# Optimization experiments

Hardware: AMD Instinct MI355X
Metric: run time of the kernel (lower is better)

The kernel has to match this reference:

```python
import jax, jax.numpy as jnp
import numpy as np

N_NODES = 100000
N_EDGES = 800000
N_ETYPES = 5
IN_DIM = 23
HID_DIM = 128
OUT_DIM = 64
NUM_GRAPHS = 64


def setup_inputs() -> dict:
    key = jax.random.key(0)
    ks = jax.random.split(key, 8)
    feat = jax.random.normal(ks[0], (N_NODES, IN_DIM), dtype=jnp.float32)
    src = jax.random.randint(ks[1], (N_ETYPES, N_EDGES), 0, N_NODES, dtype=jnp.int32)
    dst = jax.random.randint(ks[2], (N_ETYPES, N_EDGES), 0, N_NODES, dtype=jnp.int32)
    graph_ids = jnp.sort(jax.random.randint(ks[3], (N_NODES,), 0, NUM_GRAPHS, dtype=jnp.int32))
    W1 = jax.random.normal(ks[4], (N_ETYPES, IN_DIM, HID_DIM), dtype=jnp.float32) * 0.1
    b1 = jnp.zeros((N_ETYPES, HID_DIM), dtype=jnp.float32)
    W2 = jax.random.normal(ks[5], (N_ETYPES, HID_DIM, OUT_DIM), dtype=jnp.float32) * 0.1
    b2 = jnp.zeros((N_ETYPES, OUT_DIM), dtype=jnp.float32)
    return {"feat": feat, "src": src, "dst": dst, "graph_ids": graph_ids,
            "W1": W1, "b1": b1, "W2": W2, "b2": b2}


def _hetero_sage_layer(h, src, dst, W, b):
    """HeteroGraphConv of SAGEConv(aggregator='gcn') summed over edge types.
    gcn aggregator: h_neigh[i] = (sum_{j->i} h[j] + h[i]) / (in_deg(i) + 1);
    per-etype output = h_neigh @ W_e + b_e; combine with sum."""
    n = h.shape[0]
    out = jnp.zeros((n, W.shape[-1]), dtype=h.dtype)
    ones_e = jnp.ones((src.shape[1],), dtype=h.dtype)
    for e in range(N_ETYPES):
        deg = jax.ops.segment_sum(ones_e, dst[e], num_segments=n)          # [N]
        agg = jax.ops.segment_sum(h[src[e]], dst[e], num_segments=n)       # [N, D]
        h_neigh = (agg + h) / (deg + 1.0)[:, None]
        out = out + h_neigh @ W[e] + b[e]
    return out


def reference(feat, src, dst, graph_ids, W1, b1, W2, b2):
    # layer 1: in_dim -> hid, relu (dropout in eval mode = identity)
    h = jax.nn.relu(_hetero_sage_layer(feat, src, dst, W1, b1))
    # layer 2: hid -> out (no activation)
    h = _hetero_sage_layer(h, src, dst, W2, b2)
    # dgl.mean_nodes: per-graph mean over nodes
    counts = jax.ops.segment_sum(jnp.ones((h.shape[0],), h.dtype), graph_ids,
                                 num_segments=NUM_GRAPHS)
    sums = jax.ops.segment_sum(h, graph_ids, num_segments=NUM_GRAPHS)
    return sums / jnp.maximum(counts, 1.0)[:, None]
```

## Files before the change

### kernel.cpp

```cpp
#include <hip/hip_runtime.h>

#define N_NODES   100000
#define N_EDGES   800000
#define N_ETYPES  5
#define IN_DIM    23
#define HID_DIM   128
#define OUT_DIM   64
#define NUM_GRAPHS 64
#define NBKT      391
#define PBLK      125
#define CHUNK     6400
#define NB_E      (N_ETYPES*NBKT)
#define BKT_CAP   3072
#define ASTR      136
#define A1STR     40


__device__ __forceinline__ unsigned short f2bf(float x) {
    unsigned u = __float_as_uint(x);
    unsigned r = (u + 0x7FFFu + ((u >> 16) & 1u)) >> 16;
    return (unsigned short)r;
}
__device__ __forceinline__ float bf2f(unsigned short h) {
    return __uint_as_float(((unsigned)h) << 16);
}

typedef __attribute__((ext_vector_type(8))) short bf16x8;
typedef __attribute__((ext_vector_type(4))) float f32x4;
typedef __attribute__((ext_vector_type(2))) float f32x2;

__global__ __launch_bounds__(256) void cvt_feat_k(const float* __restrict__ feat,
                                                  unsigned short* __restrict__ fb8) {
    int i = blockIdx.x * 256 + threadIdx.x;
    if (i < N_NODES * 16) {
        int n = i >> 4, p = i & 15;
        int d0 = p * 2, d1 = d0 + 1;
        float f0 = (d0 < IN_DIM) ? feat[n * IN_DIM + d0] : 0.f;
        float f1 = (d1 < IN_DIM) ? feat[n * IN_DIM + d1] : 0.f;
        int pk = __builtin_amdgcn_cvt_pk_fp8_f32(f0, f1, 0, false);
        fb8[i] = (unsigned short)(pk & 0xFFFF);
    }
}

__global__ __launch_bounds__(256) void cvt_w_k(const float* __restrict__ W1,
                                               const float* __restrict__ b1,
                                               const float* __restrict__ W2,
                                               unsigned short* __restrict__ w1tb,
                                               unsigned short* __restrict__ w2tb,
                                               float* __restrict__ b1s) {
    int i = blockIdx.x * 256 + threadIdx.x;
    if (i < N_ETYPES * OUT_DIM * HID_DIM) {
        int e = i / (OUT_DIM * HID_DIM);
        int r = i - e * (OUT_DIM * HID_DIM);
        int n = r >> 7, k = r & 127;
        w2tb[i] = f2bf(W2[(e * HID_DIM + k) * OUT_DIM + n]);
    }
    if (i < N_ETYPES * HID_DIM * 32) {
        int e = i / (HID_DIM * 32);
        int r = i - e * (HID_DIM * 32);
        int n = r >> 5, k = r & 31;
        w1tb[i] = (k < IN_DIM) ? f2bf(W1[e * IN_DIM * HID_DIM + k * HID_DIM + n])
                               : (unsigned short)0;
    }
    if (i < HID_DIM) {
        float s = 0.f;
        for (int e = 0; e < N_ETYPES; e++) s += b1[e * HID_DIM + i];
        b1s[i] = s;
    }
}

__global__ __launch_bounds__(256) void part_k(const int* __restrict__ src,
                                              const int* __restrict__ dst,
                                              int* __restrict__ gcur,
                                              unsigned* __restrict__ ep) {
    __shared__ int hist[NBKT];
    __shared__ int cur[NBKT];
    int e = blockIdx.y, blk = blockIdx.x, t = threadIdx.x;
    for (int b = t; b < NBKT; b += 256) hist[b] = 0;
    __syncthreads();
    const int* dp = dst + e * N_EDGES + blk * CHUNK;
    const int* sp = src + e * N_EDGES + blk * CHUNK;
    for (int k = t; k < CHUNK; k += 256) atomicAdd(&hist[dp[k] >> 8], 1);
    __syncthreads();
    for (int b = t; b < NBKT; b += 256)
        cur[b] = (hist[b] > 0) ? atomicAdd(&gcur[e * NBKT + b], hist[b]) : 0;
    __syncthreads();
    for (int k = t; k < CHUNK; k += 256) {
        int d = dp[k], s = sp[k];
        int b = d >> 8;
        int pos = atomicAdd(&cur[b], 1);
        if (pos < BKT_CAP)
            ep[(size_t)(e * NBKT + b) * BKT_CAP + pos] =
                (unsigned)s | ((unsigned)(d & 255) << 24);
    }
}

__global__ __launch_bounds__(256) void sort_k(const int* __restrict__ gcur,
                                              const unsigned* __restrict__ ep,
                                              unsigned* __restrict__ csr,
                                              int* __restrict__ noff,
                                              int* __restrict__ degn,
                                              float* __restrict__ inv) {
    __shared__ unsigned recs[BKT_CAP];
    __shared__ int hist[256];
    __shared__ int scn[256];
    __shared__ int curp[256];
    int b = blockIdx.x, e = blockIdx.y, t = threadIdx.x;
    int lin = e * NBKT + b;
    int S = lin * BKT_CAP;
    int cnt = gcur[lin];
    if (cnt > BKT_CAP) cnt = BKT_CAP;
    hist[t] = 0;
    __syncthreads();
    for (int i = t; i < cnt; i += 256) {
        unsigned r = ep[S + i];
        recs[i] = r;
        atomicAdd(&hist[r >> 24], 1);
    }
    __syncthreads();
    scn[t] = hist[t];
    __syncthreads();
    for (int o = 1; o < 256; o <<= 1) {
        int x = (t >= o) ? scn[t - o] : 0;
        __syncthreads();
        scn[t] += x;
        __syncthreads();
    }
    int excl = scn[t] - hist[t];
    curp[t] = excl;
    int n = b * 256 + t;
    if (n < N_NODES) {
        noff[e * N_NODES + n] = S + excl;
        degn[e * N_NODES + n] = hist[t];
        inv[e * N_NODES + n]  = 1.f / (float)(hist[t] + 1);
    }
    __syncthreads();
    for (int i = t; i < cnt; i += 256) {
        unsigned r = recs[i];
        int pos = atomicAdd(&curp[r >> 24], 1);
        csr[S + pos] = r & 0xFFFFFFu;
    }
}

__global__ __launch_bounds__(256) void agg1_k(const int* __restrict__ noff,
                                              const int* __restrict__ degn,
                                              const unsigned* __restrict__ csr,
                                              const unsigned short* __restrict__ fb8,
                                              const float* __restrict__ inv,
                                              unsigned short* __restrict__ agg1b) {
    int e = blockIdx.y;
    int t = threadIdx.x;
    int lane = t & 15;
    int n = blockIdx.x * 16 + (t >> 4);
    int idx = e * N_NODES + n;
    int st = noff[idx];
    int cnt = degn[idx];
    f32x2 sv = __builtin_amdgcn_cvt_pk_f32_fp8((int)fb8[n * 16 + lane], false);
    float a0 = sv.x, a1 = sv.y;
    int k = 0;
    for (; k + 3 < cnt; k += 4) {
        int s0 = csr[st + k];
        int s1 = csr[st + k + 1];
        int s2 = csr[st + k + 2];
        int s3 = csr[st + k + 3];
        unsigned short r0 = fb8[s0 * 16 + lane];
        unsigned short r1 = fb8[s1 * 16 + lane];
        unsigned short r2 = fb8[s2 * 16 + lane];
        unsigned short r3 = fb8[s3 * 16 + lane];
        f32x2 v0 = __builtin_amdgcn_cvt_pk_f32_fp8((int)r0, false);
        f32x2 v1 = __builtin_amdgcn_cvt_pk_f32_fp8((int)r1, false);
        f32x2 v2 = __builtin_amdgcn_cvt_pk_f32_fp8((int)r2, false);
        f32x2 v3 = __builtin_amdgcn_cvt_pk_f32_fp8((int)r3, false);
        a0 += (v0.x + v1.x) + (v2.x + v3.x);
        a1 += (v0.y + v1.y) + (v2.y + v3.y);
    }
    for (; k < cnt; k++) {
        int s0 = csr[st + k];
        f32x2 v0 = __builtin_amdgcn_cvt_pk_f32_fp8((int)fb8[s0 * 16 + lane], false);
        a0 += v0.x;
        a1 += v0.y;
    }
    float iv = inv[idx];
    ushort2 o; o.x = f2bf(a0 * iv); o.y = f2bf(a1 * iv);
    *(ushort2*)&agg1b[(size_t)idx * 32 + lane * 2] = o;
}

__global__ __launch_bounds__(256) void gemm12_k(const unsigned short* __restrict__ agg1b,
                                                const unsigned short* __restrict__ w1tb,
                                                const float* __restrict__ b1s,
                                                const unsigned short* __restrict__ w2tb,
                                                unsigned char* __restrict__ t2f8) {
    __shared__ unsigned short H1s[64 * ASTR];
    __shared__ unsigned short Wt2[64 * ASTR];
    unsigned short* As1 = Wt2;
    unsigned short* Wt1 = Wt2 + 64 * A1STR;
    int t = threadIdx.x;
    int node0 = blockIdx.x * 64;
    int w = t >> 6, lane = t & 63;
    int m = lane & 15, quad = lane >> 4;

    f32x4 acc[8];
    for (int nt = 0; nt < 8; nt++) {
        float bb = b1s[nt * 16 + m];
        f32x4 c = {bb, bb, bb, bb};
        acc[nt] = c;
    }
    for (int e = 0; e < N_ETYPES; e++) {
        __syncthreads();
        for (int j = t; j < 64 * 8; j += 256) {
            int n = j >> 3, c4 = (j & 7) * 4;
            int gn = node0 + n;
            int cn = gn < N_NODES ? gn : N_NODES - 1;
            *(ushort4*)&As1[n * A1STR + c4] =
                *(const ushort4*)&agg1b[(size_t)(e * N_NODES + cn) * 32 + c4];
        }
        for (int j = t; j < 128 * 8; j += 256) {
            int n = j >> 3, c4 = (j & 7) * 4;
            *(ushort4*)&Wt1[n * A1STR + c4] =
                *(const ushort4*)&w1tb[(size_t)(e * HID_DIM + n) * 32 + c4];
        }
        __syncthreads();
        bf16x8 a = *(const bf16x8*)&As1[(w * 16 + m) * A1STR + quad * 8];
        for (int nt = 0; nt < 8; nt++) {
            bf16x8 b = *(const bf16x8*)&Wt1[(nt * 16 + m) * A1STR + quad * 8];
            acc[nt] = __builtin_amdgcn_mfma_f32_16x16x32_bf16(a, b, acc[nt], 0, 0, 0);
        }
    }
    __syncthreads();
    for (int nt = 0; nt < 8; nt++)
        for (int r = 0; r < 4; r++)
            H1s[(w * 16 + quad * 4 + r) * ASTR + nt * 16 + m] =
                f2bf(fmaxf(acc[nt][r], 0.f));
    __syncthreads();

    bf16x8 a2[4];
    for (int ks = 0; ks < 4; ks++)
        a2[ks] = *(const bf16x8*)&H1s[(w * 16 + m) * ASTR + ks * 32 + quad * 8];
    for (int e = 0; e < N_ETYPES; e++) {
        __syncthreads();
        for (int j = t; j < 64 * 32; j += 256) {
            int n = j >> 5, c4 = (j & 31) * 4;
            *(ushort4*)&Wt2[n * ASTR + c4] =
                *(const ushort4*)&w2tb[(e * OUT_DIM + n) * HID_DIM + c4];
        }
        __syncthreads();
        unsigned char* out = t2f8 + (size_t)e * N_NODES * OUT_DIM;
        for (int nt = 0; nt < 4; nt++) {
            f32x4 c = {0.f, 0.f, 0.f, 0.f};
            for (int ks = 0; ks < 4; ks++) {
                bf16x8 b = *(const bf16x8*)&Wt2[(nt * 16 + m) * ASTR + ks * 32 + quad * 8];
                c = __builtin_amdgcn_mfma_f32_16x16x32_bf16(a2[ks], b, c, 0, 0, 0);
            }
            for (int r = 0; r < 4; r++) {
                int gn = node0 + w * 16 + quad * 4 + r;
                if (gn < N_NODES) {
                    int p = __builtin_amdgcn_cvt_pk_fp8_f32(c[r], c[r], 0, false);
                    out[(size_t)gn * OUT_DIM + nt * 16 + m] = (unsigned char)(p & 0xFF);
                }
            }
        }
    }
}

__global__ __launch_bounds__(256) void gather2_k(const int* __restrict__ noff,
                                                 const int* __restrict__ degn,
                                                 const float* __restrict__ inv,
                                                 const unsigned* __restrict__ csr,
                                                 const unsigned char* __restrict__ t2f8,
                                                 const int* __restrict__ gid,
                                                 float* __restrict__ gsum) {
    __shared__ float4 red4[16 * 4 * 16];
    int b = blockIdx.x, qb = blockIdx.y, t = threadIdx.x;
    int lane = t & 15, ng = t >> 4;
    int nbase = b * 256 + qb * 32;
    int gbase = nbase < N_NODES ? nbase : N_NODES - 1;
    int g0 = gid[gbase];
    float4 f[2];
    f[0] = make_float4(0.f, 0.f, 0.f, 0.f);
    f[1] = make_float4(0.f, 0.f, 0.f, 0.f);

    for (int e = 0; e < N_ETYPES; e++) {
        const unsigned char* base = t2f8 + (size_t)e * N_NODES * OUT_DIM;
        #pragma unroll
        for (int pass = 0; pass < 2; pass++) {
            int n = nbase + pass * 16 + ng;
            if (n >= N_NODES) break;
            int idx = e * N_NODES + n;
            int st = noff[idx];
            int cnt = degn[idx];
            float iv = inv[idx];
            unsigned rv = *(const unsigned*)&base[(size_t)n * OUT_DIM + lane * 4];
            f32x2 lo = __builtin_amdgcn_cvt_pk_f32_fp8((int)rv, false);
            f32x2 hi = __builtin_amdgcn_cvt_pk_f32_fp8((int)rv, true);
            float ax = lo.x, ay = lo.y, az = hi.x, aw = hi.y;
            int k = 0;
            for (; k + 3 < cnt; k += 4) {
                int sA = csr[st + k];
                int sB = csr[st + k + 1];
                int sC = csr[st + k + 2];
                int sD = csr[st + k + 3];
                unsigned rA = *(const unsigned*)&base[(size_t)sA * OUT_DIM + lane * 4];
                unsigned rB = *(const unsigned*)&base[(size_t)sB * OUT_DIM + lane * 4];
                unsigned rC = *(const unsigned*)&base[(size_t)sC * OUT_DIM + lane * 4];
                unsigned rD = *(const unsigned*)&base[(size_t)sD * OUT_DIM + lane * 4];
                f32x2 lA = __builtin_amdgcn_cvt_pk_f32_fp8((int)rA, false);
                f32x2 hA = __builtin_amdgcn_cvt_pk_f32_fp8((int)rA, true);
                f32x2 lB = __builtin_amdgcn_cvt_pk_f32_fp8((int)rB, false);
                f32x2 hB = __builtin_amdgcn_cvt_pk_f32_fp8((int)rB, true);
                f32x2 lC = __builtin_amdgcn_cvt_pk_f32_fp8((int)rC, false);
                f32x2 hC = __builtin_amdgcn_cvt_pk_f32_fp8((int)rC, true);
                f32x2 lD = __builtin_amdgcn_cvt_pk_f32_fp8((int)rD, false);
                f32x2 hD = __builtin_amdgcn_cvt_pk_f32_fp8((int)rD, true);
                ax += (lA.x + lB.x) + (lC.x + lD.x);
                ay += (lA.y + lB.y) + (lC.y + lD.y);
                az += (hA.x + hB.x) + (hC.x + hD.x);
                aw += (hA.y + hB.y) + (hC.y + hD.y);
            }
            for (; k < cnt; k++) {
                int sA = csr[st + k];
                unsigned rA = *(const unsigned*)&base[(size_t)sA * OUT_DIM + lane * 4];
                f32x2 lA = __builtin_amdgcn_cvt_pk_f32_fp8((int)rA, false);
                f32x2 hA = __builtin_amdgcn_cvt_pk_f32_fp8((int)rA, true);
                ax += lA.x; ay += lA.y; az += hA.x; aw += hA.y;
            }
            f[pass].x += iv * ax; f[pass].y += iv * ay;
            f[pass].z += iv * az; f[pass].w += iv * aw;
        }
    }

    float4 sa0 = {0,0,0,0}, sa1 = {0,0,0,0}, sa2 = {0,0,0,0}, sa3 = {0,0,0,0};
    #pragma unroll
    for (int pass = 0; pass < 2; pass++) {
        int n = nbase + pass * 16 + ng;
        if (n >= N_NODES) break;
        float4 v = f[pass];
        int slot = gid[n] - g0;
        float m0 = (slot == 0) ? 1.f : 0.f;
        float m1 = (slot == 1) ? 1.f : 0.f;
        float m2 = (slot == 2) ? 1.f : 0.f;
        float m3 = (slot == 3) ? 1.f : 0.f;
        sa0.x += m0 * v.x; sa0.y += m0 * v.y; sa0.z += m0 * v.z; sa0.w += m0 * v.w;
        sa1.x += m1 * v.x; sa1.y += m1 * v.y; sa1.z += m1 * v.z; sa1.w += m1 * v.w;
        sa2.x += m2 * v.x; sa2.y += m2 * v.y; sa2.z += m2 * v.z; sa2.w += m2 * v.w;
        sa3.x += m3 * v.x; sa3.y += m3 * v.y; sa3.z += m3 * v.z; sa3.w += m3 * v.w;
        if (slot > 3) {
            atomicAdd(&gsum[(g0 + slot) * 64 + lane * 4 + 0], v.x);
            atomicAdd(&gsum[(g0 + slot) * 64 + lane * 4 + 1], v.y);
            atomicAdd(&gsum[(g0 + slot) * 64 + lane * 4 + 2], v.z);
            atomicAdd(&gsum[(g0 + slot) * 64 + lane * 4 + 3], v.w);
        }
    }
    red4[(ng * 4 + 0) * 16 + lane] = sa0;
    red4[(ng * 4 + 1) * 16 + lane] = sa1;
    red4[(ng * 4 + 2) * 16 + lane] = sa2;
    red4[(ng * 4 + 3) * 16 + lane] = sa3;
    __syncthreads();
    const float* red = (const float*)red4;
    int slot = t >> 6, d = t & 63;
    float s = 0.f;
    for (int j = 0; j < 16; j++) s += red[(j * 4 + slot) * 64 + d];
    int g = g0 + slot;
    if (g < NUM_GRAPHS) atomicAdd(&gsum[g * 64 + d], s);
}

__global__ __launch_bounds__(256) void gcnt_k(const int* __restrict__ gid,
                                              float* __restrict__ gcnt) {
    __shared__ int h[NUM_GRAPHS];
    int b = blockIdx.x, t = threadIdx.x;
    if (t < NUM_GRAPHS) h[t] = 0;
    __syncthreads();
    int n = b * 256 + t;
    if (n < N_NODES) atomicAdd(&h[gid[n]], 1);
    __syncthreads();
    if (t < NUM_GRAPHS && h[t] > 0) atomicAdd(&gcnt[t], (float)h[t]);
}

__global__ __launch_bounds__(256) void final_k(const float* __restrict__ gsum,
                                               const float* __restrict__ gcnt,
                                               const float* __restrict__ b2,
                                               float* __restrict__ out) {
    int idx = blockIdx.x * 256 + threadIdx.x;
    if (idx >= NUM_GRAPHS * OUT_DIM) return;
    int d = idx & 63;
    float B2 = 0.f;
    for (int e = 0; e < N_ETYPES; e++) B2 += b2[e * OUT_DIM + d];
    float c = gcnt[idx >> 6];
    out[idx] = (gsum[idx] + c * B2) / fmaxf(c, 1.0f);
}

extern "C" void kernel_launch(void* const* d_in, const int* in_sizes, int n_in,
                              void* d_out, int out_size, void* d_ws, size_t ws_size,
                              hipStream_t stream) {
    const float* feat = (const float*)d_in[0];
    const int*   src  = (const int*)d_in[1];
    const int*   dst  = (const int*)d_in[2];
    const int*   gid  = (const int*)d_in[3];
    const float* W1   = (const float*)d_in[4];
    const float* b1   = (const float*)d_in[5];
    const float* W2   = (const float*)d_in[6];
    const float* b2   = (const float*)d_in[7];

    float* ws = (float*)d_ws;
    int*            GCUR = (int*)ws;
    float*          INV  = ws + 2048;
    int*            NOFF = (int*)ws + 502048;
    int*            DEGN = (int*)ws + 1002048;
    unsigned short* FB8  = (unsigned short*)(ws + 1502048);
    float*          GSUM = ws + 2302048;
    float*          GCNT = ws + 2306144;
    unsigned*       EP   = (unsigned*)(ws + 2306208);
    unsigned*       CSR  = (unsigned*)(ws + 8311968);
    unsigned short* AGG1B= (unsigned short*)(ws + 14317728);
    unsigned char*  T2F8 = (unsigned char*)(ws + 22317728);
    unsigned short* W1TB = (unsigned short*)(ws + 30317728);
    unsigned short* W2TB = (unsigned short*)(ws + 30327968);
    float*          B1S  = ws + 30348448;

    hipMemsetAsync(GCUR, 0, 2048 * sizeof(int), stream);
    hipMemsetAsync(GSUM, 0, (size_t)(4096 + 64) * sizeof(float), stream);

    cvt_feat_k<<<(N_NODES * 16 + 255) / 256, 256, 0, stream>>>(feat, FB8);
    cvt_w_k<<<(N_ETYPES * OUT_DIM * HID_DIM + 255) / 256, 256, 0, stream>>>(
        W1, b1, W2, W1TB, W2TB, B1S);
    part_k<<<dim3(PBLK, N_ETYPES), 256, 0, stream>>>(src, dst, GCUR, EP);
    sort_k<<<dim3(NBKT, N_ETYPES), 256, 0, stream>>>(GCUR, EP, CSR, NOFF, DEGN, INV);

    agg1_k<<<dim3(6250, N_ETYPES), 256, 0, stream>>>(NOFF, DEGN, CSR, FB8, INV, AGG1B);
    gemm12_k<<<(N_NODES + 63) / 64, 256, 0, stream>>>(AGG1B, W1TB, B1S, W2TB, T2F8);
    gather2_k<<<dim3(NBKT, 8), 256, 0, stream>>>(NOFF, DEGN, INV, CSR, T2F8, gid, GSUM);

    gcnt_k<<<391, 256, 0, stream>>>(gid, GCNT);
    final_k<<<16, 256, 0, stream>>>(GSUM, GCNT, b2, (float*)d_out);
}
```

Baseline: 385.7 us.

## Fuse layer-1 neighbor aggregation into the GEMM kernel, dropping AGG1B buffer

Removes the separate agg1_k kernel and performs the fp8 feature gather and mean directly into shared memory inside gemm12_k, per edge type. This eliminates writing and re-reading the bf16 aggregated buffer (5×100k×32 bf16) and one kernel launch. In exchange, the gather latency now sits inside the GEMM kernel with only 1563 blocks, each 16-thread group serially handling 4 nodes, so latency hiding and parallelism for the irregular gather are reduced.

```diff
diff --git a/kernel.cpp b/kernel.cpp
--- a/kernel.cpp
+++ b/kernel.cpp
@@ -142,50 +142,11 @@
     }
 }
 
-__global__ __launch_bounds__(256) void agg1_k(const int* __restrict__ noff,
-                                              const int* __restrict__ degn,
-                                              const unsigned* __restrict__ csr,
-                                              const unsigned short* __restrict__ fb8,
-                                              const float* __restrict__ inv,
-                                              unsigned short* __restrict__ agg1b) {
-    int e = blockIdx.y;
-    int t = threadIdx.x;
-    int lane = t & 15;
-    int n = blockIdx.x * 16 + (t >> 4);
-    int idx = e * N_NODES + n;
-    int st = noff[idx];
-    int cnt = degn[idx];
-    f32x2 sv = __builtin_amdgcn_cvt_pk_f32_fp8((int)fb8[n * 16 + lane], false);
-    float a0 = sv.x, a1 = sv.y;
-    int k = 0;
-    for (; k + 3 < cnt; k += 4) {
-        int s0 = csr[st + k];
-        int s1 = csr[st + k + 1];
-        int s2 = csr[st + k + 2];
-        int s3 = csr[st + k + 3];
-        unsigned short r0 = fb8[s0 * 16 + lane];
-        unsigned short r1 = fb8[s1 * 16 + lane];
-        unsigned short r2 = fb8[s2 * 16 + lane];
-        unsigned short r3 = fb8[s3 * 16 + lane];
-        f32x2 v0 = __builtin_amdgcn_cvt_pk_f32_fp8((int)r0, false);
-        f32x2 v1 = __builtin_amdgcn_cvt_pk_f32_fp8((int)r1, false);
-        f32x2 v2 = __builtin_amdgcn_cvt_pk_f32_fp8((int)r2, false);
-        f32x2 v3 = __builtin_amdgcn_cvt_pk_f32_fp8((int)r3, false);
-        a0 += (v0.x + v1.x) + (v2.x + v3.x);
-        a1 += (v0.y + v1.y) + (v2.y + v3.y);
-    }
-    for (; k < cnt; k++) {
-        int s0 = csr[st + k];
-        f32x2 v0 = __builtin_amdgcn_cvt_pk_f32_fp8((int)fb8[s0 * 16 + lane], false);
-        a0 += v0.x;
-        a1 += v0.y;
-    }
-    float iv = inv[idx];
-    ushort2 o; o.x = f2bf(a0 * iv); o.y = f2bf(a1 * iv);
-    *(ushort2*)&agg1b[(size_t)idx * 32 + lane * 2] = o;
-}
-
-__global__ __launch_bounds__(256) void gemm12_k(const unsigned short* __restrict__ agg1b,
+__global__ __launch_bounds__(256) void gemm12_k(const int* __restrict__ noff,
+                                                const int* __restrict__ degn,
+                                                const float* __restrict__ inv,
+                                                const unsigned* __restrict__ csr,
+                                                const unsigned short* __restrict__ fb8,
                                                 const unsigned short* __restrict__ w1tb,
                                                 const float* __restrict__ b1s,
                                                 const unsigned short* __restrict__ w2tb,
@@ -198,6 +159,7 @@
     int node0 = blockIdx.x * 64;
     int w = t >> 6, lane = t & 63;
     int m = lane & 15, quad = lane >> 4;
+    int glane = t & 15, grp = t >> 4;
 
     f32x4 acc[8];
     for (int nt = 0; nt < 8; nt++) {
@@ -207,12 +169,37 @@
     }
     for (int e = 0; e < N_ETYPES; e++) {
         __syncthreads();
-        for (int j = t; j < 64 * 8; j += 256) {
-            int n = j >> 3, c4 = (j & 7) * 4;
-            int gn = node0 + n;
+        for (int i = 0; i < 4; i++) {
+            int nl = grp * 4 + i;
+            int gn = node0 + nl;
             int cn = gn < N_NODES ? gn : N_NODES - 1;
-            *(ushort4*)&As1[n * A1STR + c4] =
-                *(const ushort4*)&agg1b[(size_t)(e * N_NODES + cn) * 32 + c4];
+            int idx = e * N_NODES + cn;
+            int st = noff[idx];
+            int cnt = degn[idx];
+            float iv = inv[idx];
+            f32x2 sv = __builtin_amdgcn_cvt_pk_f32_fp8((int)fb8[cn * 16 + glane], false);
+            float a0 = sv.x, a1 = sv.y;
+            int k = 0;
+            for (; k + 3 < cnt; k += 4) {
+                int s0 = csr[st + k];
+                int s1 = csr[st + k + 1];
+                int s2 = csr[st + k + 2];
+                int s3 = csr[st + k + 3];
+                f32x2 v0 = __builtin_amdgcn_cvt_pk_f32_fp8((int)fb8[s0 * 16 + glane], false);
+                f32x2 v1 = __builtin_amdgcn_cvt_pk_f32_fp8((int)fb8[s1 * 16 + glane], false);
+                f32x2 v2 = __builtin_amdgcn_cvt_pk_f32_fp8((int)fb8[s2 * 16 + glane], false);
+                f32x2 v3 = __builtin_amdgcn_cvt_pk_f32_fp8((int)fb8[s3 * 16 + glane], false);
+                a0 += (v0.x + v1.x) + (v2.x + v3.x);
+                a1 += (v0.y + v1.y) + (v2.y + v3.y);
+            }
+            for (; k < cnt; k++) {
+                int s0 = csr[st + k];
+                f32x2 v0 = __builtin_amdgcn_cvt_pk_f32_fp8((int)fb8[s0 * 16 + glane], false);
+                a0 += v0.x;
+                a1 += v0.y;
+            }
+            ushort2 o; o.x = f2bf(a0 * iv); o.y = f2bf(a1 * iv);
+            *(ushort2*)&As1[nl * A1STR + glane * 2] = o;
         }
         for (int j = t; j < 128 * 8; j += 256) {
             int n = j >> 3, c4 = (j & 7) * 4;
@@ -410,11 +397,10 @@
     float*          GCNT = ws + 2306144;
     unsigned*       EP   = (unsigned*)(ws + 2306208);
     unsigned*       CSR  = (unsigned*)(ws + 8311968);
-    unsigned short* AGG1B= (unsigned short*)(ws + 14317728);
-    unsigned char*  T2F8 = (unsigned char*)(ws + 22317728);
-    unsigned short* W1TB = (unsigned short*)(ws + 30317728);
-    unsigned short* W2TB = (unsigned short*)(ws + 30327968);
-    float*          B1S  = ws + 30348448;
+    unsigned char*  T2F8 = (unsigned char*)(ws + 14317728);
+    unsigned short* W1TB = (unsigned short*)(ws + 22317728);
+    unsigned short* W2TB = (unsigned short*)(ws + 22327968);
+    float*          B1S  = ws + 22348448;
 
     hipMemsetAsync(GCUR, 0, 2048 * sizeof(int), stream);
     hipMemsetAsync(GSUM, 0, (size_t)(4096 + 64) * sizeof(float), stream);
@@ -425,8 +411,8 @@
     part_k<<<dim3(PBLK, N_ETYPES), 256, 0, stream>>>(src, dst, GCUR, EP);
     sort_k<<<dim3(NBKT, N_ETYPES), 256, 0, stream>>>(GCUR, EP, CSR, NOFF, DEGN, INV);
 
-    agg1_k<<<dim3(6250, N_ETYPES), 256, 0, stream>>>(NOFF, DEGN, CSR, FB8, INV, AGG1B);
-    gemm12_k<<<(N_NODES + 63) / 64, 256, 0, stream>>>(AGG1B, W1TB, B1S, W2TB, T2F8);
+    gemm12_k<<<(N_NODES + 63) / 64, 256, 0, stream>>>(NOFF, DEGN, INV, CSR, FB8,
+                                                      W1TB, B1S, W2TB, T2F8);
     gather2_k<<<dim3(NBKT, 8), 256, 0, stream>>>(NOFF, DEGN, INV, CSR, T2F8, gid, GSUM);
 
     gcnt_k<<<391, 256, 0, stream>>>(gid, GCNT);
```

New measurement: 401.3 us. +4.1%, slower.

## Fuse layer-1 neighbor aggregation into bucket sort kernel and merge conversion kernels

Applied to the files above, without the earlier changes.

The per-bucket sort kernel now keeps the sorted source indices in shared memory and runs the layer-1 fp8 feature aggregation for its 256 destination nodes right away, instead of launching a separate aggregation kernel that reloads CSR offsets, degrees and indices from global memory. The feature and weight conversion kernels are merged into one launch. This removes two launches and the global reads of CSR, offsets and degrees in the aggregation step. In exchange, parallelism for aggregation drops from 31250 blocks to 1955 blocks, and the extra shared-memory array may lower occupancy.

```diff
diff --git a/kernel.cpp b/kernel.cpp
--- a/kernel.cpp
+++ b/kernel.cpp
@@ -29,8 +29,14 @@
 typedef __attribute__((ext_vector_type(4))) float f32x4;
 typedef __attribute__((ext_vector_type(2))) float f32x2;
 
-__global__ __launch_bounds__(256) void cvt_feat_k(const float* __restrict__ feat,
-                                                  unsigned short* __restrict__ fb8) {
+__global__ __launch_bounds__(256) void cvt_k(const float* __restrict__ feat,
+                                             const float* __restrict__ W1,
+                                             const float* __restrict__ b1,
+                                             const float* __restrict__ W2,
+                                             unsigned short* __restrict__ fb8,
+                                             unsigned short* __restrict__ w1tb,
+                                             unsigned short* __restrict__ w2tb,
+                                             float* __restrict__ b1s) {
     int i = blockIdx.x * 256 + threadIdx.x;
     if (i < N_NODES * 16) {
         int n = i >> 4, p = i & 15;
@@ -40,15 +46,6 @@
         int pk = __builtin_amdgcn_cvt_pk_fp8_f32(f0, f1, 0, false);
         fb8[i] = (unsigned short)(pk & 0xFFFF);
     }
-}
-
-__global__ __launch_bounds__(256) void cvt_w_k(const float* __restrict__ W1,
-                                               const float* __restrict__ b1,
-                                               const float* __restrict__ W2,
-                                               unsigned short* __restrict__ w1tb,
-                                               unsigned short* __restrict__ w2tb,
-                                               float* __restrict__ b1s) {
-    int i = blockIdx.x * 256 + threadIdx.x;
     if (i < N_ETYPES * OUT_DIM * HID_DIM) {
         int e = i / (OUT_DIM * HID_DIM);
         int r = i - e * (OUT_DIM * HID_DIM);
@@ -95,16 +92,21 @@
     }
 }
 
-__global__ __launch_bounds__(256) void sort_k(const int* __restrict__ gcur,
-                                              const unsigned* __restrict__ ep,
-                                              unsigned* __restrict__ csr,
-                                              int* __restrict__ noff,
-                                              int* __restrict__ degn,
-                                              float* __restrict__ inv) {
+__global__ __launch_bounds__(256) void aggsort_k(const int* __restrict__ gcur,
+                                                 const unsigned* __restrict__ ep,
+                                                 unsigned* __restrict__ csr,
+                                                 int* __restrict__ noff,
+                                                 int* __restrict__ degn,
+                                                 float* __restrict__ inv,
+                                                 const unsigned short* __restrict__ fb8,
+                                                 unsigned short* __restrict__ agg1b) {
     __shared__ unsigned recs[BKT_CAP];
+    __shared__ unsigned srt[BKT_CAP];
     __shared__ int hist[256];
     __shared__ int scn[256];
     __shared__ int curp[256];
+    __shared__ int boffl[256];
+    __shared__ float invl[256];
     int b = blockIdx.x, e = blockIdx.y, t = threadIdx.x;
     int lin = e * NBKT + b;
     int S = lin * BKT_CAP;
@@ -128,61 +130,58 @@
     }
     int excl = scn[t] - hist[t];
     curp[t] = excl;
+    boffl[t] = excl;
+    float iv = 1.f / (float)(hist[t] + 1);
+    invl[t] = iv;
     int n = b * 256 + t;
     if (n < N_NODES) {
         noff[e * N_NODES + n] = S + excl;
         degn[e * N_NODES + n] = hist[t];
-        inv[e * N_NODES + n]  = 1.f / (float)(hist[t] + 1);
+        inv[e * N_NODES + n]  = iv;
     }
     __syncthreads();
     for (int i = t; i < cnt; i += 256) {
         unsigned r = recs[i];
         int pos = atomicAdd(&curp[r >> 24], 1);
-        csr[S + pos] = r & 0xFFFFFFu;
-    }
-}
-
-__global__ __launch_bounds__(256) void agg1_k(const int* __restrict__ noff,
-                                              const int* __restrict__ degn,
-                                              const unsigned* __restrict__ csr,
-                                              const unsigned short* __restrict__ fb8,
-                                              const float* __restrict__ inv,
-                                              unsigned short* __restrict__ agg1b) {
-    int e = blockIdx.y;
-    int t = threadIdx.x;
-    int lane = t & 15;
-    int n = blockIdx.x * 16 + (t >> 4);
-    int idx = e * N_NODES + n;
-    int st = noff[idx];
-    int cnt = degn[idx];
-    f32x2 sv = __builtin_amdgcn_cvt_pk_f32_fp8((int)fb8[n * 16 + lane], false);
-    float a0 = sv.x, a1 = sv.y;
-    int k = 0;
-    for (; k + 3 < cnt; k += 4) {
-        int s0 = csr[st + k];
-        int s1 = csr[st + k + 1];
-        int s2 = csr[st + k + 2];
-        int s3 = csr[st + k + 3];
-        unsigned short r0 = fb8[s0 * 16 + lane];
-        unsigned short r1 = fb8[s1 * 16 + lane];
-        unsigned short r2 = fb8[s2 * 16 + lane];
-        unsigned short r3 = fb8[s3 * 16 + lane];
-        f32x2 v0 = __builtin_amdgcn_cvt_pk_f32_fp8((int)r0, false);
-        f32x2 v1 = __builtin_amdgcn_cvt_pk_f32_fp8((int)r1, false);
-        f32x2 v2 = __builtin_amdgcn_cvt_pk_f32_fp8((int)r2, false);
-        f32x2 v3 = __builtin_amdgcn_cvt_pk_f32_fp8((int)r3, false);
-        a0 += (v0.x + v1.x) + (v2.x + v3.x);
-        a1 += (v0.y + v1.y) + (v2.y + v3.y);
-    }
-    for (; k < cnt; k++) {
-        int s0 = csr[st + k];
-        f32x2 v0 = __builtin_amdgcn_cvt_pk_f32_fp8((int)fb8[s0 * 16 + lane], false);
-        a0 += v0.x;
-        a1 += v0.y;
-    }
-    float iv = inv[idx];
-    ushort2 o; o.x = f2bf(a0 * iv); o.y = f2bf(a1 * iv);
-    *(ushort2*)&agg1b[(size_t)idx * 32 + lane * 2] = o;
+        srt[pos] = r & 0xFFFFFFu;
+    }
+    __syncthreads();
+    for (int i = t; i < cnt; i += 256) csr[S + i] = srt[i];
+
+    int glane = t & 15, grp = t >> 4;
+    for (int pass = 0; pass < 16; pass++) {
+        int nl = pass * 16 + grp;
+        int gn = b * 256 + nl;
+        int cn = gn < N_NODES ? gn : N_NODES - 1;
+        int st = boffl[nl];
+        int dn = hist[nl];
+        f32x2 sv = __builtin_amdgcn_cvt_pk_f32_fp8((int)fb8[cn * 16 + glane], false);
+        float a0 = sv.x, a1 = sv.y;
+        int k = 0;
+        for (; k + 3 < dn; k += 4) {
+            int s0 = srt[st + k];
+            int s1 = srt[st + k + 1];
+            int s2 = srt[st + k + 2];
+            int s3 = srt[st + k + 3];
+            f32x2 v0 = __builtin_amdgcn_cvt_pk_f32_fp8((int)fb8[s0 * 16 + glane], false);
+            f32x2 v1 = __builtin_amdgcn_cvt_pk_f32_fp8((int)fb8[s1 * 16 + glane], false);
+            f32x2 v2 = __builtin_amdgcn_cvt_pk_f32_fp8((int)fb8[s2 * 16 + glane], false);
+            f32x2 v3 = __builtin_amdgcn_cvt_pk_f32_fp8((int)fb8[s3 * 16 + glane], false);
+            a0 += (v0.x + v1.x) + (v2.x + v3.x);
+            a1 += (v0.y + v1.y) + (v2.y + v3.y);
+        }
+        for (; k < dn; k++) {
+            int s0 = srt[st + k];
+            f32x2 v0 = __builtin_amdgcn_cvt_pk_f32_fp8((int)fb8[s0 * 16 + glane], false);
+            a0 += v0.x;
+            a1 += v0.y;
+        }
+        if (gn < N_NODES) {
+            float ivv = invl[nl];
+            ushort2 o; o.x = f2bf(a0 * ivv); o.y = f2bf(a1 * ivv);
+            *(ushort2*)&agg1b[(size_t)(e * N_NODES + gn) * 32 + glane * 2] = o;
+        }
+    }
 }
 
 __global__ __launch_bounds__(256) void gemm12_k(const unsigned short* __restrict__ agg1b,
@@ -419,13 +418,11 @@
     hipMemsetAsync(GCUR, 0, 2048 * sizeof(int), stream);
     hipMemsetAsync(GSUM, 0, (size_t)(4096 + 64) * sizeof(float), stream);
 
-    cvt_feat_k<<<(N_NODES * 16 + 255) / 256, 256, 0, stream>>>(feat, FB8);
-    cvt_w_k<<<(N_ETYPES * OUT_DIM * HID_DIM + 255) / 256, 256, 0, stream>>>(
-        W1, b1, W2, W1TB, W2TB, B1S);
+    cvt_k<<<(N_NODES * 16 + 255) / 256, 256, 0, stream>>>(feat, W1, b1, W2,
+                                                          FB8, W1TB, W2TB, B1S);
     part_k<<<dim3(PBLK, N_ETYPES), 256, 0, stream>>>(src, dst, GCUR, EP);
-    sort_k<<<dim3(NBKT, N_ETYPES), 256, 0, stream>>>(GCUR, EP, CSR, NOFF, DEGN, INV);
-
-    agg1_k<<<dim3(6250, N_ETYPES), 256, 0, stream>>>(NOFF, DEGN, CSR, FB8, INV, AGG1B);
+    aggsort_k<<<dim3(NBKT, N_ETYPES), 256, 0, stream>>>(GCUR, EP, CSR, NOFF, DEGN,
+                                                        INV, FB8, AGG1B);
     gemm12_k<<<(N_NODES + 63) / 64, 256, 0, stream>>>(AGG1B, W1TB, B1S, W2TB, T2F8);
     gather2_k<<<dim3(NBKT, 8), 256, 0, stream>>>(NOFF, DEGN, INV, CSR, T2F8, gid, GSUM);
 
```

After: 363.5 us. 5.8% less time.
